# Kernel optimization log

Hardware: AMD Instinct MI355X
Metric: run time of the kernel (lower is better)

Reference implementation:

```python
import jax, jax.numpy as jnp
import numpy as np

M, N, K, C, G = 16384, 131072, 16, 128, 8
EPS_BN = 1e-5


def _bn(x, g, b):
    # inference-mode BatchNorm1d (running_mean=0, running_var=1)
    return x * (g / jnp.sqrt(1.0 + EPS_BN)) + b


def setup_inputs() -> dict:
    key = jax.random.key(0)
    ks = jax.random.split(key, 16)
    f32 = jnp.float32
    s = 0.05
    return {
        "query_feat": jax.random.normal(ks[0], (M, C), f32),
        "context_feat": jax.random.normal(ks[1], (N, C), f32),
        "query_coord": jax.random.normal(ks[2], (M, 3), f32),
        "context_coord": jax.random.normal(ks[3], (N, 3), f32),
        "Wq": jax.random.normal(ks[4], (C, C), f32) * s,
        "bq": jnp.zeros((C,), f32),
        "gq": jnp.ones((C,), f32),
        "betaq": jnp.zeros((C,), f32),
        "Wk": jax.random.normal(ks[5], (C, C), f32) * s,
        "bk": jnp.zeros((C,), f32),
        "gk": jnp.ones((C,), f32),
        "betak": jnp.zeros((C,), f32),
        "Wv": jax.random.normal(ks[6], (C, C), f32) * s,
        "bv": jnp.zeros((C,), f32),
        "Wp1": jax.random.normal(ks[7], (3, C), f32) * s,
        "bp1": jnp.zeros((C,), f32),
        "gp1": jnp.ones((C,), f32),
        "betap1": jnp.zeros((C,), f32),
        "Wp2": jax.random.normal(ks[8], (C, C), f32) * s,
        "bp2": jnp.zeros((C,), f32),
        "Ww1": jax.random.normal(ks[9], (C, G), f32) * s,
        "bw1": jnp.zeros((G,), f32),
        "gw1": jnp.ones((G,), f32),
        "betaw1": jnp.zeros((G,), f32),
        "Ww2": jax.random.normal(ks[10], (G, G), f32) * s,
        "bw2": jnp.zeros((G,), f32),
        "knn_indexes": jax.random.randint(ks[11], (M, K), 0, N, dtype=jnp.int32),
    }


def reference(query_feat, context_feat, query_coord, context_coord,
              Wq, bq, gq, betaq, Wk, bk, gk, betak, Wv, bv,
              Wp1, bp1, gp1, betap1, Wp2, bp2,
              Ww1, bw1, gw1, betaw1, Ww2, bw2, knn_indexes):
    q = jax.nn.relu(_bn(query_feat @ Wq + bq, gq, betaq))              # (M, C)
    k = jax.nn.relu(_bn(context_feat @ Wk + bk, gk, betak))            # (N, C)
    v = context_feat @ Wv + bv                                         # (N, C)

    mask = knn_indexes >= 0                                            # (M, K); -1 = padded neighbor
    idx = jnp.where(mask, knn_indexes, 0)
    mf = mask[..., None].astype(q.dtype)                               # (M, K, 1)

    key_g = k[idx] * mf                                                # (M, K, C) gather (zero row for -1)
    val_g = v[idx] * mf                                                # (M, K, C)
    pos = (context_coord[idx] - query_coord[:, None, :]) * mf          # (M, K, 3) relative position

    # positional-encoding bias branch (pe_bias=True, pe_multiplier=False)
    peb = jax.nn.relu(_bn(pos @ Wp1 + bp1, gp1, betap1)) @ Wp2 + bp2   # (M, K, C)
    rel = key_g - q[:, None, :] + peb                                  # (M, K, C)
    val_g = val_g + peb

    # grouped vector attention weights
    w = jax.nn.relu(_bn(rel @ Ww1 + bw1, gw1, betaw1)) @ Ww2 + bw2     # (M, K, G)
    w = jax.nn.softmax(w, axis=1) * mf                                 # softmax over neighbors, mask padded

    m_, k_ = idx.shape
    c_ = q.shape[-1]
    g_ = w.shape[-1]
    out = jnp.einsum('mkgi,mkg->mgi', val_g.reshape(m_, k_, g_, c_ // g_), w)
    return out.reshape(m_, c_)
```

## Files before the change

kernel.cpp:

```cpp
#include <hip/hip_runtime.h>

#define C 128
#define G 8
#define KNN 16
#define QB 4
#define EPS 1e-5f

typedef unsigned short u16;
typedef __attribute__((ext_vector_type(8))) short short8;
typedef __attribute__((ext_vector_type(4))) float float4v;

union frag_u { short8 v; u16 u[8]; };

__device__ inline u16 f2bf(float f) {
    unsigned u = __builtin_bit_cast(unsigned, f);
    unsigned r = (u + 0x7fffu + ((u >> 16) & 1u)) >> 16;
    return (u16)r;
}
__device__ inline float bf2f(u16 h) {
    unsigned u = ((unsigned)h) << 16;
    return __builtin_bit_cast(float, u);
}

__global__ __launch_bounds__(256) void prep_w(
    const float* __restrict__ Wk, const float* __restrict__ Wv,
    const float* __restrict__ Wq, const float* __restrict__ Wp2,
    const float* __restrict__ Ww1, const float* __restrict__ bp2,
    u16* __restrict__ dst, float* __restrict__ cw1)
{
    const int b = blockIdx.x, t = threadIdx.x;
    if (b < 16) {
        const int mi = b >> 2, qt = b & 3;
        const float* W = mi == 0 ? Wk : mi == 1 ? Wv : mi == 2 ? Wq : Wp2;
        u16* d = dst + mi * 16384;
        for (int e = qt * 4096 + t; e < (qt + 1) * 4096; e += 256) {
            const int k = e >> 7, n = e & 127;
            const int cb = n >> 4, lan = n & 15;
            const int kk = k >> 5, quad = (k >> 3) & 3, j = k & 7;
            d[(((cb * 4 + kk) * 4 + quad) * 16 + lan) * 8 + j] = f2bf(W[e]);
        }
    } else if (b == 16) {
        u16* d = dst + 4 * 16384;
        for (int e = t; e < 4096; e += 256) {
            const int j = e & 7, lan = (e >> 3) & 15;
            const int quad = (e >> 7) & 3, kk = e >> 9;
            const int k = kk * 32 + quad * 8 + j;
            d[e] = lan < 8 ? f2bf(Ww1[k * G + lan]) : (u16)0;
        }
    } else {
        u16* d = dst + 4 * 16384 + 4096;
        for (int e = t; e < 4096; e += 256) d[e] = 0;
        __syncthreads();
#pragma unroll
        for (int it = 0; it < 4; it++) {
            const int k = it * 32 + (t >> 3), g = t & 7;
            float a = 0.f;
            for (int i = 0; i < C; i++)
                a = fmaf(Wp2[k * C + i], Ww1[i * G + g], a);
            const int kk = k >> 5, quad = (k >> 3) & 3, j = k & 7;
            d[((kk * 4 + quad) * 16 + g) * 8 + j] = f2bf(a);
        }
        if (t < G) {
            float a = 0.f;
            for (int i = 0; i < C; i++) a = fmaf(bp2[i], Ww1[i * G + t], a);
            cw1[t] = a;
        }
    }
}

__global__ __launch_bounds__(256) void proj_all(
    const float* __restrict__ Xc, const float* __restrict__ Xq,
    const u16* __restrict__ PWk, const float* __restrict__ bk,
    const float* __restrict__ gk, const float* __restrict__ betak,
    const u16* __restrict__ PWv, const float* __restrict__ bv,
    const u16* __restrict__ PWq, const float* __restrict__ bq,
    const float* __restrict__ gq, const float* __restrict__ betaq,
    const u16* __restrict__ PWw1b,
    u16* __restrict__ vout, u16* __restrict__ Kp, u16* __restrict__ Qp,
    int nkv)
{
    __shared__ u16 Xs[64 * 136];
    const int t = threadIdx.x;
    const int w = t >> 6, l = t & 63;
    const int quad = l >> 4, lan = l & 15;
    const bool isq = (int)blockIdx.x >= nkv;
    const long long row0 = (long long)(isq ? blockIdx.x - nkv : blockIdx.x) * 64;
    const float* X = isq ? Xq : Xc;

    {
        const float4* Xv = (const float4*)(X + row0 * C);
#pragma unroll
        for (int i = 0; i < 8; i++) {
            const int e = t + 256 * i;
            const int r = e >> 5, c4 = e & 31;
            const float4 f = Xv[e];
            uint2 p;
            p.x = (unsigned)f2bf(f.x) | ((unsigned)f2bf(f.y) << 16);
            p.y = (unsigned)f2bf(f.z) | ((unsigned)f2bf(f.w) << 16);
            *(uint2*)(&Xs[r * 136 + c4 * 4]) = p;
        }
    }
    __syncthreads();

    if (!isq) {
        unsigned vp[2][4][2];
        {
            short8 Bf[2][4];
#pragma unroll
            for (int ct = 0; ct < 2; ct++) {
                const int cb = w * 2 + ct;
#pragma unroll
                for (int kk = 0; kk < 4; kk++)
                    Bf[ct][kk] = *(const short8*)(PWv + (((cb * 4 + kk) * 4 + quad) * 16 + lan) * 8);
            }
            float4v acc[2][4];
#pragma unroll
            for (int ct = 0; ct < 2; ct++)
#pragma unroll
                for (int rt = 0; rt < 4; rt++) acc[ct][rt] = (float4v)0.f;
#pragma unroll
            for (int rt = 0; rt < 4; rt++)
#pragma unroll
                for (int kk = 0; kk < 4; kk++) {
                    const short8 A = *(const short8*)(&Xs[(rt * 16 + lan) * 136 + kk * 32 + quad * 8]);
#pragma unroll
                    for (int ct = 0; ct < 2; ct++)
                        acc[ct][rt] = __builtin_amdgcn_mfma_f32_16x16x32_bf16(
                            A, Bf[ct][kk], acc[ct][rt], 0, 0, 0);
                }
#pragma unroll
            for (int ct = 0; ct < 2; ct++) {
                const float bb = bv[w * 32 + ct * 16 + lan];
#pragma unroll
                for (int rt = 0; rt < 4; rt++)
#pragma unroll
                    for (int h = 0; h < 2; h++)
                        vp[ct][rt][h] = (unsigned)f2bf(acc[ct][rt][2 * h] + bb)
                                      | ((unsigned)f2bf(acc[ct][rt][2 * h + 1] + bb) << 16);
            }
        }
        float4v acck[2][4];
        {
            short8 Bf[2][4];
#pragma unroll
            for (int ct = 0; ct < 2; ct++) {
                const int cb = w * 2 + ct;
#pragma unroll
                for (int kk = 0; kk < 4; kk++)
                    Bf[ct][kk] = *(const short8*)(PWk + (((cb * 4 + kk) * 4 + quad) * 16 + lan) * 8);
            }
#pragma unroll
            for (int ct = 0; ct < 2; ct++)
#pragma unroll
                for (int rt = 0; rt < 4; rt++) acck[ct][rt] = (float4v)0.f;
#pragma unroll
            for (int rt = 0; rt < 4; rt++)
#pragma unroll
                for (int kk = 0; kk < 4; kk++) {
                    const short8 A = *(const short8*)(&Xs[(rt * 16 + lan) * 136 + kk * 32 + quad * 8]);
#pragma unroll
                    for (int ct = 0; ct < 2; ct++)
                        acck[ct][rt] = __builtin_amdgcn_mfma_f32_16x16x32_bf16(
                            A, Bf[ct][kk], acck[ct][rt], 0, 0, 0);
                }
        }
        __syncthreads();

#pragma unroll
        for (int ct = 0; ct < 2; ct++) {
            const int cg = w * 32 + ct * 16 + lan;
            const float bb = bk[cg];
            const float sc = gk[cg] * rsqrtf(1.f + EPS);
            const float sh = betak[cg];
#pragma unroll
            for (int rt = 0; rt < 4; rt++)
#pragma unroll
                for (int reg = 0; reg < 4; reg++) {
                    float y = (acck[ct][rt][reg] + bb) * sc + sh;
                    y = y > 0.f ? y : 0.f;
                    Xs[(rt * 16 + quad * 4 + reg) * 136 + cg] = f2bf(y);
                }
        }
        __syncthreads();

        {
            short8 Bw[4];
#pragma unroll
            for (int kk = 0; kk < 4; kk++)
                Bw[kk] = *(const short8*)(PWw1b + ((kk * 4 + quad) * 16 + lan) * 8);
            float4v ka = (float4v)0.f;
#pragma unroll
            for (int kk = 0; kk < 4; kk++) {
                const short8 A = *(const short8*)(&Xs[(w * 16 + lan) * 136 + kk * 32 + quad * 8]);
                ka = __builtin_amdgcn_mfma_f32_16x16x32_bf16(A, Bw[kk], ka, 0, 0, 0);
            }
            if (lan < G) {
#pragma unroll
                for (int reg = 0; reg < 4; reg++)
                    Kp[(row0 + w * 16 + quad * 4 + reg) * G + lan] = f2bf(ka[reg]);
            }
        }
        __syncthreads();

#pragma unroll
        for (int ct = 0; ct < 2; ct++) {
            const int cg = w * 32 + ct * 16 + lan;
#pragma unroll
            for (int rt = 0; rt < 4; rt++)
#pragma unroll
                for (int h = 0; h < 2; h++) {
                    Xs[(rt * 16 + quad * 4 + 2 * h) * 136 + cg]     = (u16)(vp[ct][rt][h] & 0xffffu);
                    Xs[(rt * 16 + quad * 4 + 2 * h + 1) * 136 + cg] = (u16)(vp[ct][rt][h] >> 16);
                }
        }
        __syncthreads();
#pragma unroll
        for (int i = 0; i < 4; i++) {
            const int e = t + 256 * i;
            const int r = e >> 4, cc = (e & 15) * 8;
            *(short8*)(vout + (row0 + r) * C + cc) = *(const short8*)(&Xs[r * 136 + cc]);
        }
    } else {
        float4v acc[2][4];
        {
            short8 Bf[2][4];
#pragma unroll
            for (int ct = 0; ct < 2; ct++) {
                const int cb = w * 2 + ct;
#pragma unroll
                for (int kk = 0; kk < 4; kk++)
                    Bf[ct][kk] = *(const short8*)(PWq + (((cb * 4 + kk) * 4 + quad) * 16 + lan) * 8);
            }
#pragma unroll
            for (int ct = 0; ct < 2; ct++)
#pragma unroll
                for (int rt = 0; rt < 4; rt++) acc[ct][rt] = (float4v)0.f;
#pragma unroll
            for (int rt = 0; rt < 4; rt++)
#pragma unroll
                for (int kk = 0; kk < 4; kk++) {
                    const short8 A = *(const short8*)(&Xs[(rt * 16 + lan) * 136 + kk * 32 + quad * 8]);
#pragma unroll
                    for (int ct = 0; ct < 2; ct++)
                        acc[ct][rt] = __builtin_amdgcn_mfma_f32_16x16x32_bf16(
                            A, Bf[ct][kk], acc[ct][rt], 0, 0, 0);
                }
        }
        __syncthreads();
#pragma unroll
        for (int ct = 0; ct < 2; ct++) {
            const int cg = w * 32 + ct * 16 + lan;
            const float bb = bq[cg];
            const float sc = gq[cg] * rsqrtf(1.f + EPS);
            const float sh = betaq[cg];
#pragma unroll
            for (int rt = 0; rt < 4; rt++)
#pragma unroll
                for (int reg = 0; reg < 4; reg++) {
                    float y = (acc[ct][rt][reg] + bb) * sc + sh;
                    y = y > 0.f ? y : 0.f;
                    Xs[(rt * 16 + quad * 4 + reg) * 136 + cg] = f2bf(y);
                }
        }
        __syncthreads();
        {
            short8 Bw[4];
#pragma unroll
            for (int kk = 0; kk < 4; kk++)
                Bw[kk] = *(const short8*)(PWw1b + ((kk * 4 + quad) * 16 + lan) * 8);
            float4v qa = (float4v)0.f;
#pragma unroll
            for (int kk = 0; kk < 4; kk++) {
                const short8 A = *(const short8*)(&Xs[(w * 16 + lan) * 136 + kk * 32 + quad * 8]);
                qa = __builtin_amdgcn_mfma_f32_16x16x32_bf16(A, Bw[kk], qa, 0, 0, 0);
            }
            if (lan < G) {
#pragma unroll
                for (int reg = 0; reg < 4; reg++)
                    Qp[(row0 + w * 16 + quad * 4 + reg) * G + lan] = f2bf(qa[reg]);
            }
        }
    }
}

__global__ __launch_bounds__(256) void attn6(
    const u16* __restrict__ vbuf, const u16* __restrict__ Kp,
    const u16* __restrict__ Qp,
    const float* __restrict__ qcoord, const float* __restrict__ ccoord,
    const float* __restrict__ Wp1, const float* __restrict__ bp1,
    const float* __restrict__ gp1, const float* __restrict__ betap1,
    const u16* __restrict__ PWp2, const float* __restrict__ bp2,
    const u16* __restrict__ PWp2pb, const float* __restrict__ cw1,
    const float* __restrict__ bw1,
    const float* __restrict__ gw1, const float* __restrict__ betaw1,
    const float* __restrict__ Ww2, const float* __restrict__ bw2,
    const int* __restrict__ knn, float* __restrict__ out)
{
    __shared__ u16   fA[64 * 136];
    __shared__ u16   kgs[64 * G];
    __shared__ float qps[QB * G];
    __shared__ float pebp[64 * G];
    __shared__ float cw1s[G];
    __shared__ float pxs[64], pys[64], pzs[64];
    __shared__ int   idxs[64];
    __shared__ float wl[QB * 16 * G];

    const int t = threadIdx.x;
    const int w = t >> 6, l = t & 63;
    const int quad = l >> 4, lan = l & 15;
    const int m0 = blockIdx.x * QB;
    const int rsub = t >> 4;
    const int c8 = (t & 15) * 8;

    float mfr[4];
    frag_u vg[4];
#pragma unroll
    for (int p = 0; p < 4; p++) {
        const int ii = knn[m0 * KNN + p * 16 + rsub];
        mfr[p] = ii >= 0 ? 1.f : 0.f;
        const size_t i0 = ii >= 0 ? ii : 0;
        vg[p].v = *(const short8*)(vbuf + i0 * C + c8);
    }
    if (t < 64) {
        const int q = t >> 4;
        const int ii = knn[m0 * KNN + t];
        const float mf = ii >= 0 ? 1.f : 0.f;
        const int i0 = ii >= 0 ? ii : 0;
        idxs[t] = ii;
        pxs[t] = (ccoord[i0 * 3 + 0] - qcoord[(m0 + q) * 3 + 0]) * mf;
        pys[t] = (ccoord[i0 * 3 + 1] - qcoord[(m0 + q) * 3 + 1]) * mf;
        pzs[t] = (ccoord[i0 * 3 + 2] - qcoord[(m0 + q) * 3 + 2]) * mf;
        *(short8*)(&kgs[t * G]) = *(const short8*)(Kp + (size_t)i0 * G);
    } else if (t < 68) {
        const int p = t - 64;
        frag_u qv;
        qv.v = *(const short8*)(Qp + (size_t)(m0 + p) * G);
#pragma unroll
        for (int j = 0; j < G; j++) qps[p * G + j] = bf2f(qv.u[j]);
    } else if (t < 76) {
        cw1s[t - 68] = cw1[t - 68];
    }
    __syncthreads();

    {
        const int c = t & 127, hh = t >> 7;
        const float w0 = Wp1[c], w1_ = Wp1[C + c], w2_ = Wp1[2 * C + c];
        const float sc = gp1[c] * rsqrtf(1.f + EPS);
        const float bb = bp1[c], sh = betap1[c];
#pragma unroll
        for (int r2 = 0; r2 < 32; r2++) {
            const int r = hh * 32 + r2;
            float y = fmaf(pxs[r], w0, fmaf(pys[r], w1_, fmaf(pzs[r], w2_, bb)));
            y = y * sc + sh;
            y = y > 0.f ? y : 0.f;
            fA[r * 136 + c] = f2bf(y);
        }
    }
    __syncthreads();

    float4v acc[2][4];
    float4v pp = (float4v)0.f;
    {
        short8 Bf[2][4];
#pragma unroll
        for (int ct = 0; ct < 2; ct++) {
            const int cb = w * 2 + ct;
#pragma unroll
            for (int kk = 0; kk < 4; kk++)
                Bf[ct][kk] = *(const short8*)(PWp2 + (((cb * 4 + kk) * 4 + quad) * 16 + lan) * 8);
        }
#pragma unroll
        for (int ct = 0; ct < 2; ct++)
#pragma unroll
            for (int q = 0; q < 4; q++) acc[ct][q] = (float4v)0.f;
#pragma unroll
        for (int q = 0; q < 4; q++)
#pragma unroll
            for (int kk = 0; kk < 4; kk++) {
                const short8 A = *(const short8*)(&fA[(q * 16 + lan) * 136 + kk * 32 + quad * 8]);
#pragma unroll
                for (int ct = 0; ct < 2; ct++)
                    acc[ct][q] = __builtin_amdgcn_mfma_f32_16x16x32_bf16(
                        A, Bf[ct][kk], acc[ct][q], 0, 0, 0);
            }
#pragma unroll
        for (int kk = 0; kk < 4; kk++) {
            const short8 Bp = *(const short8*)(PWp2pb + ((kk * 4 + quad) * 16 + lan) * 8);
            const short8 A = *(const short8*)(&fA[(w * 16 + lan) * 136 + kk * 32 + quad * 8]);
            pp = __builtin_amdgcn_mfma_f32_16x16x32_bf16(A, Bp, pp, 0, 0, 0);
        }
    }
    __syncthreads();

    {
        const float bb0 = bp2[w * 32 + lan];
        const float bb1 = bp2[w * 32 + 16 + lan];
#pragma unroll
        for (int ct = 0; ct < 2; ct++)
#pragma unroll
            for (int q = 0; q < 4; q++)
#pragma unroll
                for (int reg = 0; reg < 4; reg++)
                    fA[(q * 16 + quad * 4 + reg) * 136 + w * 32 + ct * 16 + lan] =
                        f2bf(acc[ct][q][reg] + (ct ? bb1 : bb0));
        if (lan < G) {
#pragma unroll
            for (int reg = 0; reg < 4; reg++)
                pebp[(w * 16 + quad * 4 + reg) * G + lan] = pp[reg];
        }
    }
    __syncthreads();

    {
#pragma unroll
        for (int p = 0; p < 4; p++) {
            const int r = p * 16 + rsub;
            const float mf = mfr[p];
            frag_u peb, valv;
            peb.v = *(const short8*)(&fA[r * 136 + c8]);
#pragma unroll
            for (int j = 0; j < 8; j++)
                valv.u[j] = f2bf(fmaf(bf2f(vg[p].u[j]), mf, bf2f(peb.u[j])));
            *(short8*)(&fA[r * 136 + c8]) = valv.v;
        }
    }
    if (t < 64) {
        const int q = t >> 4, j = t & 15;
        const float mf = idxs[t] >= 0 ? 1.f : 0.f;
#pragma unroll
        for (int g = 0; g < G; g++) {
            const float L = bf2f(kgs[t * G + g]) * mf - qps[q * G + g]
                          + pebp[t * G + g] + cw1s[g] + bw1[g];
            const float y = L * (gw1[g] * rsqrtf(1.f + EPS)) + betaw1[g];
            wl[q * 128 + j * G + g] = y > 0.f ? y : 0.f;
        }
    }
    __syncthreads();

    if (t < QB * G) {
        const int q = t >> 3, g2 = t & 7;
        float w2c[G];
#pragma unroll
        for (int g = 0; g < G; g++) w2c[g] = Ww2[g * G + g2];
        const float bb = bw2[g2];
        float lg[KNN], mx = -1e30f;
#pragma unroll
        for (int j = 0; j < KNN; j++) {
            float a = bb;
#pragma unroll
            for (int g = 0; g < G; g++) a = fmaf(wl[q * 128 + j * 8 + g], w2c[g], a);
            lg[j] = a;
            mx = fmaxf(mx, a);
        }
        float sum = 0.f;
#pragma unroll
        for (int j = 0; j < KNN; j++) { lg[j] = __expf(lg[j] - mx); sum += lg[j]; }
        const float inv = 1.f / sum;
#pragma unroll
        for (int j = 0; j < KNN; j++) {
            const float mf = idxs[q * 16 + j] >= 0 ? 1.f : 0.f;
            wl[q * 128 + j * 8 + g2] = lg[j] * inv * mf;
        }
    }
    __syncthreads();

#pragma unroll
    for (int i = 0; i < 2; i++) {
        const int e = t + 256 * i;
        const int q = e >> 7, c = e & 127, g = c >> 4;
        float a = 0.f;
#pragma unroll
        for (int j = 0; j < KNN; j++)
            a = fmaf(bf2f(fA[(q * 16 + j) * 136 + c]), wl[q * 128 + j * 8 + g], a);
        out[(size_t)(m0 + q) * C + c] = a;
    }
}

extern "C" void kernel_launch(void* const* d_in, const int* in_sizes, int n_in,
                              void* d_out, int out_size, void* d_ws, size_t ws_size,
                              hipStream_t stream)
{
    const float* query_feat    = (const float*)d_in[0];
    const float* context_feat  = (const float*)d_in[1];
    const float* query_coord   = (const float*)d_in[2];
    const float* context_coord = (const float*)d_in[3];
    const float* Wq    = (const float*)d_in[4];
    const float* bq    = (const float*)d_in[5];
    const float* gq    = (const float*)d_in[6];
    const float* betaq = (const float*)d_in[7];
    const float* Wk    = (const float*)d_in[8];
    const float* bk    = (const float*)d_in[9];
    const float* gk    = (const float*)d_in[10];
    const float* betak = (const float*)d_in[11];
    const float* Wv    = (const float*)d_in[12];
    const float* bv    = (const float*)d_in[13];
    const float* Wp1   = (const float*)d_in[14];
    const float* bp1   = (const float*)d_in[15];
    const float* gp1   = (const float*)d_in[16];
    const float* betap1= (const float*)d_in[17];
    const float* Wp2   = (const float*)d_in[18];
    const float* bp2   = (const float*)d_in[19];
    const float* Ww1   = (const float*)d_in[20];
    const float* bw1   = (const float*)d_in[21];
    const float* gw1   = (const float*)d_in[22];
    const float* betaw1= (const float*)d_in[23];
    const float* Ww2   = (const float*)d_in[24];
    const float* bw2   = (const float*)d_in[25];
    const int*   knn   = (const int*)d_in[26];

    const int M = in_sizes[0] / C;
    const int N = in_sizes[1] / C;

    u16* vb = (u16*)d_ws;
    u16* Kp = vb + (size_t)N * C;
    u16* Qp = Kp + (size_t)N * G;
    u16* pw = Qp + (size_t)M * G;
    u16* pWk    = pw;
    u16* pWv    = pw + 16384;
    u16* pWq    = pw + 2 * 16384;
    u16* pWp2   = pw + 3 * 16384;
    u16* pWw1b  = pw + 4 * 16384;
    u16* pWp2pb = pw + 4 * 16384 + 4096;
    float* cw1  = (float*)(pw + 4 * 16384 + 2 * 4096);

    prep_w<<<18, 256, 0, stream>>>(Wk, Wv, Wq, Wp2, Ww1, bp2, pw, cw1);
    proj_all<<<N / 64 + M / 64, 256, 0, stream>>>(
        context_feat, query_feat,
        pWk, bk, gk, betak, pWv, bv,
        pWq, bq, gq, betaq, pWw1b,
        vb, Kp, Qp, N / 64);
    attn6<<<M / QB, 256, 0, stream>>>(vb, Kp, Qp, query_coord, context_coord,
                                      Wp1, bp1, gp1, betap1, pWp2, bp2,
                                      pWp2pb, cw1, bw1, gw1, betaw1, Ww2, bw2,
                                      knn, (float*)d_out);
}
```

Measured before the change: 218.8 us.

## Compute positional first layer with MFMA and pack bf16 conversions

The 3->128 positional-encoding linear layer in the attention kernel now runs as a zero-padded bf16 MFMA, using a new prepacked Wp1 fragment built by an extra prep block, in place of scalar FMAs over LDS coordinates. Shared memory is overlaid so the position buffer, pebp and wl share one region, which adds a sync. Scalar bf16 rounding is replaced by packed float2->bf16 intrinsics in several places. This cuts VALU work and LDS footprint, at the cost of padding waste in the MFMA and bf16 rounding of the coordinates and Wp1.

```diff
diff --git a/kernel.cpp b/kernel.cpp
--- a/kernel.cpp
+++ b/kernel.cpp
@@ -1,4 +1,5 @@
 #include <hip/hip_runtime.h>
+#include <hip/hip_bf16.h>
 
 #define C 128
 #define G 8
@@ -10,7 +11,7 @@
 typedef __attribute__((ext_vector_type(8))) short short8;
 typedef __attribute__((ext_vector_type(4))) float float4v;
 
-union frag_u { short8 v; u16 u[8]; };
+union frag_u { short8 v; u16 u[8]; unsigned d[4]; };
 
 __device__ inline u16 f2bf(float f) {
     unsigned u = __builtin_bit_cast(unsigned, f);
@@ -21,11 +22,18 @@
     unsigned u = ((unsigned)h) << 16;
     return __builtin_bit_cast(float, u);
 }
+__device__ inline unsigned pkbf(float a, float b) {
+    __hip_bfloat162 h = __float22bfloat162_rn(float2{a, b});
+    unsigned r;
+    __builtin_memcpy(&r, &h, 4);
+    return r;
+}
 
 __global__ __launch_bounds__(256) void prep_w(
     const float* __restrict__ Wk, const float* __restrict__ Wv,
     const float* __restrict__ Wq, const float* __restrict__ Wp2,
-    const float* __restrict__ Ww1, const float* __restrict__ bp2,
+    const float* __restrict__ Ww1, const float* __restrict__ Wp1,
+    const float* __restrict__ bp2,
     u16* __restrict__ dst, float* __restrict__ cw1)
 {
     const int b = blockIdx.x, t = threadIdx.x;
@@ -47,7 +55,7 @@
             const int k = kk * 32 + quad * 8 + j;
             d[e] = lan < 8 ? f2bf(Ww1[k * G + lan]) : (u16)0;
         }
-    } else {
+    } else if (b == 17) {
         u16* d = dst + 4 * 16384 + 4096;
         for (int e = t; e < 4096; e += 256) d[e] = 0;
         __syncthreads();
@@ -64,6 +72,16 @@
             float a = 0.f;
             for (int i = 0; i < C; i++) a = fmaf(bp2[i], Ww1[i * G + t], a);
             cw1[t] = a;
+        }
+    } else {
+        u16* d = dst + 4 * 16384 + 2 * 4096;
+        for (int e = t; e < 4096; e += 256) d[e] = 0;
+        __syncthreads();
+        if (t < 128) {
+            const int cb = t >> 4, lan = t & 15;
+#pragma unroll
+            for (int j = 0; j < 3; j++)
+                d[(cb * 64 + lan) * 8 + j] = f2bf(Wp1[j * C + cb * 16 + lan]);
         }
     }
 }
@@ -79,7 +97,7 @@
     u16* __restrict__ vout, u16* __restrict__ Kp, u16* __restrict__ Qp,
     int nkv)
 {
-    __shared__ u16 Xs[64 * 136];
+    __shared__ __align__(16) u16 Xs[64 * 136];
     const int t = threadIdx.x;
     const int w = t >> 6, l = t & 63;
     const int quad = l >> 4, lan = l & 15;
@@ -95,8 +113,8 @@
             const int r = e >> 5, c4 = e & 31;
             const float4 f = Xv[e];
             uint2 p;
-            p.x = (unsigned)f2bf(f.x) | ((unsigned)f2bf(f.y) << 16);
-            p.y = (unsigned)f2bf(f.z) | ((unsigned)f2bf(f.w) << 16);
+            p.x = pkbf(f.x, f.y);
+            p.y = pkbf(f.z, f.w);
             *(uint2*)(&Xs[r * 136 + c4 * 4]) = p;
         }
     }
@@ -135,8 +153,7 @@
                 for (int rt = 0; rt < 4; rt++)
 #pragma unroll
                     for (int h = 0; h < 2; h++)
-                        vp[ct][rt][h] = (unsigned)f2bf(acc[ct][rt][2 * h] + bb)
-                                      | ((unsigned)f2bf(acc[ct][rt][2 * h + 1] + bb) << 16);
+                        vp[ct][rt][h] = pkbf(acc[ct][rt][2 * h] + bb, acc[ct][rt][2 * h + 1] + bb);
             }
         }
         float4v acck[2][4];
@@ -283,11 +300,11 @@
     }
 }
 
-__global__ __launch_bounds__(256) void attn6(
+__global__ __launch_bounds__(256) void attn7(
     const u16* __restrict__ vbuf, const u16* __restrict__ Kp,
     const u16* __restrict__ Qp,
     const float* __restrict__ qcoord, const float* __restrict__ ccoord,
-    const float* __restrict__ Wp1, const float* __restrict__ bp1,
+    const u16* __restrict__ PWp1b, const float* __restrict__ bp1,
     const float* __restrict__ gp1, const float* __restrict__ betap1,
     const u16* __restrict__ PWp2, const float* __restrict__ bp2,
     const u16* __restrict__ PWp2pb, const float* __restrict__ cw1,
@@ -296,14 +313,15 @@
     const float* __restrict__ Ww2, const float* __restrict__ bw2,
     const int* __restrict__ knn, float* __restrict__ out)
 {
-    __shared__ u16   fA[64 * 136];
-    __shared__ u16   kgs[64 * G];
+    __shared__ __align__(16) u16 fA[64 * 136];
+    __shared__ __align__(16) float ovl[1024];
+    __shared__ __align__(16) u16 kgs[64 * G];
     __shared__ float qps[QB * G];
-    __shared__ float pebp[64 * G];
     __shared__ float cw1s[G];
-    __shared__ float pxs[64], pys[64], pzs[64];
     __shared__ int   idxs[64];
-    __shared__ float wl[QB * 16 * G];
+    u16*   posb = (u16*)ovl;
+    float* pebp = ovl;
+    float* wl   = ovl + 512;
 
     const int t = threadIdx.x;
     const int w = t >> 6, l = t & 63;
@@ -327,9 +345,16 @@
         const float mf = ii >= 0 ? 1.f : 0.f;
         const int i0 = ii >= 0 ? ii : 0;
         idxs[t] = ii;
-        pxs[t] = (ccoord[i0 * 3 + 0] - qcoord[(m0 + q) * 3 + 0]) * mf;
-        pys[t] = (ccoord[i0 * 3 + 1] - qcoord[(m0 + q) * 3 + 1]) * mf;
-        pzs[t] = (ccoord[i0 * 3 + 2] - qcoord[(m0 + q) * 3 + 2]) * mf;
+        const float px = (ccoord[i0 * 3 + 0] - qcoord[(m0 + q) * 3 + 0]) * mf;
+        const float py = (ccoord[i0 * 3 + 1] - qcoord[(m0 + q) * 3 + 1]) * mf;
+        const float pz = (ccoord[i0 * 3 + 2] - qcoord[(m0 + q) * 3 + 2]) * mf;
+        frag_u z; z.v = (short8)0;
+        z.u[0] = f2bf(px); z.u[1] = f2bf(py); z.u[2] = f2bf(pz);
+        const short8 zz = (short8)0;
+        *(short8*)(&posb[t * 32])      = z.v;
+        *(short8*)(&posb[t * 32 + 8])  = zz;
+        *(short8*)(&posb[t * 32 + 16]) = zz;
+        *(short8*)(&posb[t * 32 + 24]) = zz;
         *(short8*)(&kgs[t * G]) = *(const short8*)(Kp + (size_t)i0 * G);
     } else if (t < 68) {
         const int p = t - 64;
@@ -343,17 +368,36 @@
     __syncthreads();
 
     {
-        const int c = t & 127, hh = t >> 7;
-        const float w0 = Wp1[c], w1_ = Wp1[C + c], w2_ = Wp1[2 * C + c];
-        const float sc = gp1[c] * rsqrtf(1.f + EPS);
-        const float bb = bp1[c], sh = betap1[c];
-#pragma unroll
-        for (int r2 = 0; r2 < 32; r2++) {
-            const int r = hh * 32 + r2;
-            float y = fmaf(pxs[r], w0, fmaf(pys[r], w1_, fmaf(pzs[r], w2_, bb)));
-            y = y * sc + sh;
-            y = y > 0.f ? y : 0.f;
-            fA[r * 136 + c] = f2bf(y);
+        short8 Bp[2];
+#pragma unroll
+        for (int ct = 0; ct < 2; ct++)
+            Bp[ct] = *(const short8*)(PWp1b + (((w * 2 + ct) * 4 + quad) * 16 + lan) * 8);
+        float4v ha[2][4];
+#pragma unroll
+        for (int ct = 0; ct < 2; ct++)
+#pragma unroll
+            for (int q = 0; q < 4; q++) ha[ct][q] = (float4v)0.f;
+#pragma unroll
+        for (int q = 0; q < 4; q++) {
+            const short8 A = *(const short8*)(&posb[(q * 16 + lan) * 32 + quad * 8]);
+#pragma unroll
+            for (int ct = 0; ct < 2; ct++)
+                ha[ct][q] = __builtin_amdgcn_mfma_f32_16x16x32_bf16(A, Bp[ct], ha[ct][q], 0, 0, 0);
+        }
+        __syncthreads();
+#pragma unroll
+        for (int ct = 0; ct < 2; ct++) {
+            const int col = w * 32 + ct * 16 + lan;
+            const float sc = gp1[col] * rsqrtf(1.f + EPS);
+            const float bb = bp1[col], sh = betap1[col];
+#pragma unroll
+            for (int q = 0; q < 4; q++)
+#pragma unroll
+                for (int reg = 0; reg < 4; reg++) {
+                    float y = (ha[ct][q][reg] + bb) * sc + sh;
+                    y = y > 0.f ? y : 0.f;
+                    fA[(q * 16 + quad * 4 + reg) * 136 + col] = f2bf(y);
+                }
         }
     }
     __syncthreads();
@@ -419,8 +463,9 @@
             frag_u peb, valv;
             peb.v = *(const short8*)(&fA[r * 136 + c8]);
 #pragma unroll
-            for (int j = 0; j < 8; j++)
-                valv.u[j] = f2bf(fmaf(bf2f(vg[p].u[j]), mf, bf2f(peb.u[j])));
+            for (int h = 0; h < 4; h++)
+                valv.d[h] = pkbf(fmaf(bf2f(vg[p].u[2 * h]),     mf, bf2f(peb.u[2 * h])),
+                                 fmaf(bf2f(vg[p].u[2 * h + 1]), mf, bf2f(peb.u[2 * h + 1])));
             *(short8*)(&fA[r * 136 + c8]) = valv.v;
         }
     }
@@ -521,16 +566,17 @@
     u16* pWp2   = pw + 3 * 16384;
     u16* pWw1b  = pw + 4 * 16384;
     u16* pWp2pb = pw + 4 * 16384 + 4096;
-    float* cw1  = (float*)(pw + 4 * 16384 + 2 * 4096);
-
-    prep_w<<<18, 256, 0, stream>>>(Wk, Wv, Wq, Wp2, Ww1, bp2, pw, cw1);
+    u16* pWp1b  = pw + 4 * 16384 + 2 * 4096;
+    float* cw1  = (float*)(pw + 4 * 16384 + 3 * 4096);
+
+    prep_w<<<19, 256, 0, stream>>>(Wk, Wv, Wq, Wp2, Ww1, Wp1, bp2, pw, cw1);
     proj_all<<<N / 64 + M / 64, 256, 0, stream>>>(
         context_feat, query_feat,
         pWk, bk, gk, betak, pWv, bv,
         pWq, bq, gq, betaq, pWw1b,
         vb, Kp, Qp, N / 64);
-    attn6<<<M / QB, 256, 0, stream>>>(vb, Kp, Qp, query_coord, context_coord,
-                                      Wp1, bp1, gp1, betap1, pWp2, bp2,
+    attn7<<<M / QB, 256, 0, stream>>>(vb, Kp, Qp, query_coord, context_coord,
+                                      pWp1b, bp1, gp1, betap1, pWp2, bp2,
                                       pWp2pb, cw1, bw1, gw1, betaw1, Ww2, bw2,
                                       knn, (float*)d_out);
 }
```

After: 220.0 us. About the same (+0.5%).

## Restructure attention kernel to one query per wave without block barriers

Applied to the files above, without the earlier changes.

The attention kernel now gives each wavefront a single query with its own shared-memory slice, so every __syncthreads is gone and softmax reductions use wave shuffles. The first positional layer (3->C linear plus BN and bias) is folded into a prepacked bf16 weight tile and computed with one MFMA per column tile, replacing scalar FMAs. Packed bf16 conversion intrinsics replace manual rounding in proj_all. Trade-offs: the Wp2 B fragments are now loaded from global memory per wave instead of being amortised across queries, and the wave-local LDS use relies on implicit in-wave ordering.

```diff
diff --git a/kernel.cpp b/kernel.cpp
--- a/kernel.cpp
+++ b/kernel.cpp
@@ -1,16 +1,16 @@
 #include <hip/hip_runtime.h>
+#include <hip/hip_bf16.h>
 
 #define C 128
 #define G 8
 #define KNN 16
-#define QB 4
 #define EPS 1e-5f
 
 typedef unsigned short u16;
 typedef __attribute__((ext_vector_type(8))) short short8;
 typedef __attribute__((ext_vector_type(4))) float float4v;
 
-union frag_u { short8 v; u16 u[8]; };
+union frag_u { short8 v; u16 u[8]; unsigned d[4]; };
 
 __device__ inline u16 f2bf(float f) {
     unsigned u = __builtin_bit_cast(unsigned, f);
@@ -21,11 +21,19 @@
     unsigned u = ((unsigned)h) << 16;
     return __builtin_bit_cast(float, u);
 }
+__device__ inline unsigned pkbf(float a, float b) {
+    __hip_bfloat162 h = __float22bfloat162_rn(float2{a, b});
+    unsigned r;
+    __builtin_memcpy(&r, &h, 4);
+    return r;
+}
 
 __global__ __launch_bounds__(256) void prep_w(
     const float* __restrict__ Wk, const float* __restrict__ Wv,
     const float* __restrict__ Wq, const float* __restrict__ Wp2,
-    const float* __restrict__ Ww1, const float* __restrict__ bp2,
+    const float* __restrict__ Ww1, const float* __restrict__ Wp1,
+    const float* __restrict__ bp1, const float* __restrict__ gp1,
+    const float* __restrict__ betap1, const float* __restrict__ bp2,
     u16* __restrict__ dst, float* __restrict__ cw1)
 {
     const int b = blockIdx.x, t = threadIdx.x;
@@ -47,7 +55,7 @@
             const int k = kk * 32 + quad * 8 + j;
             d[e] = lan < 8 ? f2bf(Ww1[k * G + lan]) : (u16)0;
         }
-    } else {
+    } else if (b == 17) {
         u16* d = dst + 4 * 16384 + 4096;
         for (int e = t; e < 4096; e += 256) d[e] = 0;
         __syncthreads();
@@ -64,6 +72,19 @@
             float a = 0.f;
             for (int i = 0; i < C; i++) a = fmaf(bp2[i], Ww1[i * G + t], a);
             cw1[t] = a;
+        }
+    } else {
+        u16* d = dst + 4 * 16384 + 2 * 4096;
+        for (int e = t; e < 4096; e += 256) d[e] = 0;
+        __syncthreads();
+        if (t < 128) {
+            const int cb = t >> 4, lan = t & 15;
+            const int col = cb * 16 + lan;
+            const float s = gp1[col] * rsqrtf(1.f + EPS);
+#pragma unroll
+            for (int j = 0; j < 3; j++)
+                d[(cb * 64 + lan) * 8 + j] = f2bf(Wp1[j * C + col] * s);
+            d[(cb * 64 + lan) * 8 + 3] = f2bf(bp1[col] * s + betap1[col]);
         }
     }
 }
@@ -79,7 +100,7 @@
     u16* __restrict__ vout, u16* __restrict__ Kp, u16* __restrict__ Qp,
     int nkv)
 {
-    __shared__ u16 Xs[64 * 136];
+    __shared__ __align__(16) u16 Xs[64 * 136];
     const int t = threadIdx.x;
     const int w = t >> 6, l = t & 63;
     const int quad = l >> 4, lan = l & 15;
@@ -95,8 +116,8 @@
             const int r = e >> 5, c4 = e & 31;
             const float4 f = Xv[e];
             uint2 p;
-            p.x = (unsigned)f2bf(f.x) | ((unsigned)f2bf(f.y) << 16);
-            p.y = (unsigned)f2bf(f.z) | ((unsigned)f2bf(f.w) << 16);
+            p.x = pkbf(f.x, f.y);
+            p.y = pkbf(f.z, f.w);
             *(uint2*)(&Xs[r * 136 + c4 * 4]) = p;
         }
     }
@@ -135,8 +156,7 @@
                 for (int rt = 0; rt < 4; rt++)
 #pragma unroll
                     for (int h = 0; h < 2; h++)
-                        vp[ct][rt][h] = (unsigned)f2bf(acc[ct][rt][2 * h] + bb)
-                                      | ((unsigned)f2bf(acc[ct][rt][2 * h + 1] + bb) << 16);
+                        vp[ct][rt][h] = pkbf(acc[ct][rt][2 * h] + bb, acc[ct][rt][2 * h + 1] + bb);
             }
         }
         float4v acck[2][4];
@@ -283,12 +303,11 @@
     }
 }
 
-__global__ __launch_bounds__(256) void attn6(
+__global__ __launch_bounds__(256) void attn8(
     const u16* __restrict__ vbuf, const u16* __restrict__ Kp,
     const u16* __restrict__ Qp,
     const float* __restrict__ qcoord, const float* __restrict__ ccoord,
-    const float* __restrict__ Wp1, const float* __restrict__ bp1,
-    const float* __restrict__ gp1, const float* __restrict__ betap1,
+    const u16* __restrict__ PWp1b,
     const u16* __restrict__ PWp2, const float* __restrict__ bp2,
     const u16* __restrict__ PWp2pb, const float* __restrict__ cw1,
     const float* __restrict__ bw1,
@@ -296,184 +315,154 @@
     const float* __restrict__ Ww2, const float* __restrict__ bw2,
     const int* __restrict__ knn, float* __restrict__ out)
 {
-    __shared__ u16   fA[64 * 136];
-    __shared__ u16   kgs[64 * G];
-    __shared__ float qps[QB * G];
-    __shared__ float pebp[64 * G];
-    __shared__ float cw1s[G];
-    __shared__ float pxs[64], pys[64], pzs[64];
-    __shared__ int   idxs[64];
-    __shared__ float wl[QB * 16 * G];
-
+    __shared__ __align__(16) unsigned char smem[4 * 5120];
     const int t = threadIdx.x;
     const int w = t >> 6, l = t & 63;
     const int quad = l >> 4, lan = l & 15;
-    const int m0 = blockIdx.x * QB;
-    const int rsub = t >> 4;
-    const int c8 = (t & 15) * 8;
-
-    float mfr[4];
+    const int m = blockIdx.x * 4 + w;
+
+    u16*   h1v = (u16*)(smem + w * 5120);
+    u16*   kg  = h1v + 16 * 136;
+    float* wl  = (float*)(kg + 16 * 8);
+
+    int ii = -1;
+    if (l < KNN) ii = knn[m * KNN + l];
+    const int myrow = l >> 2;
+    const int idxr = __shfl(ii, myrow);
+    const float mfrow = idxr >= 0 ? 1.f : 0.f;
+    const size_t r0 = idxr >= 0 ? (size_t)idxr : 0;
+    const int c0 = (l & 3) * 32;
+
     frag_u vg[4];
 #pragma unroll
-    for (int p = 0; p < 4; p++) {
-        const int ii = knn[m0 * KNN + p * 16 + rsub];
-        mfr[p] = ii >= 0 ? 1.f : 0.f;
-        const size_t i0 = ii >= 0 ? ii : 0;
-        vg[p].v = *(const short8*)(vbuf + i0 * C + c8);
-    }
-    if (t < 64) {
-        const int q = t >> 4;
-        const int ii = knn[m0 * KNN + t];
+    for (int h = 0; h < 4; h++)
+        vg[h].v = *(const short8*)(vbuf + r0 * C + c0 + h * 8);
+
+    float px = 0.f, py = 0.f, pz = 0.f;
+    if (l < KNN) {
+        const int i0 = ii >= 0 ? ii : 0;
         const float mf = ii >= 0 ? 1.f : 0.f;
-        const int i0 = ii >= 0 ? ii : 0;
-        idxs[t] = ii;
-        pxs[t] = (ccoord[i0 * 3 + 0] - qcoord[(m0 + q) * 3 + 0]) * mf;
-        pys[t] = (ccoord[i0 * 3 + 1] - qcoord[(m0 + q) * 3 + 1]) * mf;
-        pzs[t] = (ccoord[i0 * 3 + 2] - qcoord[(m0 + q) * 3 + 2]) * mf;
-        *(short8*)(&kgs[t * G]) = *(const short8*)(Kp + (size_t)i0 * G);
-    } else if (t < 68) {
-        const int p = t - 64;
-        frag_u qv;
-        qv.v = *(const short8*)(Qp + (size_t)(m0 + p) * G);
-#pragma unroll
-        for (int j = 0; j < G; j++) qps[p * G + j] = bf2f(qv.u[j]);
-    } else if (t < 76) {
-        cw1s[t - 68] = cw1[t - 68];
-    }
-    __syncthreads();
-
-    {
-        const int c = t & 127, hh = t >> 7;
-        const float w0 = Wp1[c], w1_ = Wp1[C + c], w2_ = Wp1[2 * C + c];
-        const float sc = gp1[c] * rsqrtf(1.f + EPS);
-        const float bb = bp1[c], sh = betap1[c];
-#pragma unroll
-        for (int r2 = 0; r2 < 32; r2++) {
-            const int r = hh * 32 + r2;
-            float y = fmaf(pxs[r], w0, fmaf(pys[r], w1_, fmaf(pzs[r], w2_, bb)));
-            y = y * sc + sh;
-            y = y > 0.f ? y : 0.f;
-            fA[r * 136 + c] = f2bf(y);
-        }
-    }
-    __syncthreads();
-
-    float4v acc[2][4];
+        px = (ccoord[i0 * 3 + 0] - qcoord[m * 3 + 0]) * mf;
+        py = (ccoord[i0 * 3 + 1] - qcoord[m * 3 + 1]) * mf;
+        pz = (ccoord[i0 * 3 + 2] - qcoord[m * 3 + 2]) * mf;
+        *(short8*)(&kg[l * G]) = *(const short8*)(Kp + (size_t)i0 * G);
+    }
+
+    frag_u A0; A0.v = (short8)0;
+    if (quad == 0) {
+        A0.u[0] = f2bf(px); A0.u[1] = f2bf(py); A0.u[2] = f2bf(pz);
+        A0.u[3] = 0x3F80;
+    }
+    float4v h1a[8];
+#pragma unroll
+    for (int ct = 0; ct < 8; ct++) {
+        const short8 Bp = *(const short8*)(PWp1b + ((ct * 4 + quad) * 16 + lan) * 8);
+        h1a[ct] = __builtin_amdgcn_mfma_f32_16x16x32_bf16(A0.v, Bp, (float4v)0.f, 0, 0, 0);
+    }
+#pragma unroll
+    for (int ct = 0; ct < 8; ct++)
+#pragma unroll
+        for (int reg = 0; reg < 4; reg++) {
+            const float y = h1a[ct][reg] > 0.f ? h1a[ct][reg] : 0.f;
+            h1v[(quad * 4 + reg) * 136 + ct * 16 + lan] = f2bf(y);
+        }
+
+    float4v pacc[8];
+#pragma unroll
+    for (int ct = 0; ct < 8; ct++) pacc[ct] = (float4v)0.f;
     float4v pp = (float4v)0.f;
-    {
-        short8 Bf[2][4];
-#pragma unroll
-        for (int ct = 0; ct < 2; ct++) {
-            const int cb = w * 2 + ct;
-#pragma unroll
-            for (int kk = 0; kk < 4; kk++)
-                Bf[ct][kk] = *(const short8*)(PWp2 + (((cb * 4 + kk) * 4 + quad) * 16 + lan) * 8);
-        }
-#pragma unroll
-        for (int ct = 0; ct < 2; ct++)
-#pragma unroll
-            for (int q = 0; q < 4; q++) acc[ct][q] = (float4v)0.f;
-#pragma unroll
-        for (int q = 0; q < 4; q++)
-#pragma unroll
-            for (int kk = 0; kk < 4; kk++) {
-                const short8 A = *(const short8*)(&fA[(q * 16 + lan) * 136 + kk * 32 + quad * 8]);
-#pragma unroll
-                for (int ct = 0; ct < 2; ct++)
-                    acc[ct][q] = __builtin_amdgcn_mfma_f32_16x16x32_bf16(
-                        A, Bf[ct][kk], acc[ct][q], 0, 0, 0);
-            }
-#pragma unroll
-        for (int kk = 0; kk < 4; kk++) {
-            const short8 Bp = *(const short8*)(PWp2pb + ((kk * 4 + quad) * 16 + lan) * 8);
-            const short8 A = *(const short8*)(&fA[(w * 16 + lan) * 136 + kk * 32 + quad * 8]);
-            pp = __builtin_amdgcn_mfma_f32_16x16x32_bf16(A, Bp, pp, 0, 0, 0);
-        }
-    }
-    __syncthreads();
-
-    {
-        const float bb0 = bp2[w * 32 + lan];
-        const float bb1 = bp2[w * 32 + 16 + lan];
-#pragma unroll
-        for (int ct = 0; ct < 2; ct++)
-#pragma unroll
-            for (int q = 0; q < 4; q++)
-#pragma unroll
-                for (int reg = 0; reg < 4; reg++)
-                    fA[(q * 16 + quad * 4 + reg) * 136 + w * 32 + ct * 16 + lan] =
-                        f2bf(acc[ct][q][reg] + (ct ? bb1 : bb0));
-        if (lan < G) {
-#pragma unroll
-            for (int reg = 0; reg < 4; reg++)
-                pebp[(w * 16 + quad * 4 + reg) * G + lan] = pp[reg];
-        }
-    }
-    __syncthreads();
-
-    {
-#pragma unroll
-        for (int p = 0; p < 4; p++) {
-            const int r = p * 16 + rsub;
-            const float mf = mfr[p];
-            frag_u peb, valv;
-            peb.v = *(const short8*)(&fA[r * 136 + c8]);
-#pragma unroll
-            for (int j = 0; j < 8; j++)
-                valv.u[j] = f2bf(fmaf(bf2f(vg[p].u[j]), mf, bf2f(peb.u[j])));
-            *(short8*)(&fA[r * 136 + c8]) = valv.v;
-        }
-    }
-    if (t < 64) {
-        const int q = t >> 4, j = t & 15;
-        const float mf = idxs[t] >= 0 ? 1.f : 0.f;
-#pragma unroll
-        for (int g = 0; g < G; g++) {
-            const float L = bf2f(kgs[t * G + g]) * mf - qps[q * G + g]
-                          + pebp[t * G + g] + cw1s[g] + bw1[g];
-            const float y = L * (gw1[g] * rsqrtf(1.f + EPS)) + betaw1[g];
-            wl[q * 128 + j * G + g] = y > 0.f ? y : 0.f;
-        }
-    }
-    __syncthreads();
-
-    if (t < QB * G) {
-        const int q = t >> 3, g2 = t & 7;
-        float w2c[G];
-#pragma unroll
-        for (int g = 0; g < G; g++) w2c[g] = Ww2[g * G + g2];
-        const float bb = bw2[g2];
-        float lg[KNN], mx = -1e30f;
-#pragma unroll
-        for (int j = 0; j < KNN; j++) {
-            float a = bb;
-#pragma unroll
-            for (int g = 0; g < G; g++) a = fmaf(wl[q * 128 + j * 8 + g], w2c[g], a);
-            lg[j] = a;
-            mx = fmaxf(mx, a);
-        }
-        float sum = 0.f;
-#pragma unroll
-        for (int j = 0; j < KNN; j++) { lg[j] = __expf(lg[j] - mx); sum += lg[j]; }
-        const float inv = 1.f / sum;
-#pragma unroll
-        for (int j = 0; j < KNN; j++) {
-            const float mf = idxs[q * 16 + j] >= 0 ? 1.f : 0.f;
-            wl[q * 128 + j * 8 + g2] = lg[j] * inv * mf;
-        }
-    }
-    __syncthreads();
-
-#pragma unroll
-    for (int i = 0; i < 2; i++) {
-        const int e = t + 256 * i;
-        const int q = e >> 7, c = e & 127, g = c >> 4;
-        float a = 0.f;
-#pragma unroll
-        for (int j = 0; j < KNN; j++)
-            a = fmaf(bf2f(fA[(q * 16 + j) * 136 + c]), wl[q * 128 + j * 8 + g], a);
-        out[(size_t)(m0 + q) * C + c] = a;
-    }
+#pragma unroll
+    for (int kk = 0; kk < 4; kk++) {
+        const short8 A = *(const short8*)(&h1v[lan * 136 + kk * 32 + quad * 8]);
+#pragma unroll
+        for (int ct = 0; ct < 8; ct++) {
+            const short8 Bf = *(const short8*)(PWp2 + (((ct * 4 + kk) * 4 + quad) * 16 + lan) * 8);
+            pacc[ct] = __builtin_amdgcn_mfma_f32_16x16x32_bf16(A, Bf, pacc[ct], 0, 0, 0);
+        }
+        const short8 Bpp = *(const short8*)(PWp2pb + ((kk * 4 + quad) * 16 + lan) * 8);
+        pp = __builtin_amdgcn_mfma_f32_16x16x32_bf16(A, Bpp, pp, 0, 0, 0);
+    }
+
+#pragma unroll
+    for (int ct = 0; ct < 8; ct++) {
+        const float bb = bp2[ct * 16 + lan];
+#pragma unroll
+        for (int reg = 0; reg < 4; reg++)
+            h1v[(quad * 4 + reg) * 136 + ct * 16 + lan] = f2bf(pacc[ct][reg] + bb);
+    }
+
+#pragma unroll
+    for (int h = 0; h < 4; h++) {
+        frag_u pe, va;
+        pe.v = *(const short8*)(&h1v[myrow * 136 + c0 + h * 8]);
+#pragma unroll
+        for (int x = 0; x < 4; x++)
+            va.d[x] = pkbf(fmaf(bf2f(vg[h].u[2 * x]),     mfrow, bf2f(pe.u[2 * x])),
+                           fmaf(bf2f(vg[h].u[2 * x + 1]), mfrow, bf2f(pe.u[2 * x + 1])));
+        *(short8*)(&h1v[myrow * 136 + c0 + h * 8]) = va.v;
+    }
+
+    const int g = lan & 7;
+    const float qpg  = bf2f(Qp[(size_t)m * G + g]);
+    const float cst  = cw1[g] + bw1[g];
+    const float sg   = gw1[g] * rsqrtf(1.f + EPS);
+    const float shg  = betaw1[g];
+    const float mfq0 = __shfl(ii, quad * 4 + 0) >= 0 ? 1.f : 0.f;
+    const float mfq1 = __shfl(ii, quad * 4 + 1) >= 0 ? 1.f : 0.f;
+    const float mfq2 = __shfl(ii, quad * 4 + 2) >= 0 ? 1.f : 0.f;
+    const float mfq3 = __shfl(ii, quad * 4 + 3) >= 0 ? 1.f : 0.f;
+    const float mfj[4] = {mfq0, mfq1, mfq2, mfq3};
+    if (lan < G) {
+#pragma unroll
+        for (int reg = 0; reg < 4; reg++) {
+            const int row = quad * 4 + reg;
+            const float kv = bf2f(kg[row * G + g]);
+            const float L = kv * mfj[reg] - qpg + pp[reg] + cst;
+            const float y = L * sg + shg;
+            wl[row * G + g] = y > 0.f ? y : 0.f;
+        }
+    }
+
+    float w2c[G];
+#pragma unroll
+    for (int gg = 0; gg < G; gg++) w2c[gg] = Ww2[gg * G + g];
+    const float bb2 = bw2[g];
+    float lg[4];
+#pragma unroll
+    for (int reg = 0; reg < 4; reg++) {
+        const int row = quad * 4 + reg;
+        float a = bb2;
+#pragma unroll
+        for (int gg = 0; gg < G; gg++) a = fmaf(wl[row * G + gg], w2c[gg], a);
+        lg[reg] = a;
+    }
+    float mx = fmaxf(fmaxf(lg[0], lg[1]), fmaxf(lg[2], lg[3]));
+    mx = fmaxf(mx, __shfl_xor(mx, 16));
+    mx = fmaxf(mx, __shfl_xor(mx, 32));
+    float e[4], s = 0.f;
+#pragma unroll
+    for (int reg = 0; reg < 4; reg++) { e[reg] = __expf(lg[reg] - mx); s += e[reg]; }
+    s += __shfl_xor(s, 16);
+    s += __shfl_xor(s, 32);
+    const float inv = 1.f / s;
+    if (lan < G) {
+#pragma unroll
+        for (int reg = 0; reg < 4; reg++)
+            wl[(quad * 4 + reg) * G + g] = e[reg] * inv * mfj[reg];
+    }
+
+    const int cpa = 2 * l;
+    const int gout = l >> 3;
+    float a0 = 0.f, a1 = 0.f;
+#pragma unroll
+    for (int j = 0; j < KNN; j++) {
+        const unsigned pv = *(const unsigned*)(&h1v[j * 136 + cpa]);
+        const float wj = wl[j * G + gout];
+        a0 = fmaf(bf2f((u16)(pv & 0xffffu)), wj, a0);
+        a1 = fmaf(bf2f((u16)(pv >> 16)), wj, a1);
+    }
+    float2 o; o.x = a0; o.y = a1;
+    *(float2*)(out + (size_t)m * C + cpa) = o;
 }
 
 extern "C" void kernel_launch(void* const* d_in, const int* in_sizes, int n_in,
@@ -521,16 +510,18 @@
     u16* pWp2   = pw + 3 * 16384;
     u16* pWw1b  = pw + 4 * 16384;
     u16* pWp2pb = pw + 4 * 16384 + 4096;
-    float* cw1  = (float*)(pw + 4 * 16384 + 2 * 4096);
-
-    prep_w<<<18, 256, 0, stream>>>(Wk, Wv, Wq, Wp2, Ww1, bp2, pw, cw1);
+    u16* pWp1b  = pw + 4 * 16384 + 2 * 4096;
+    float* cw1  = (float*)(pw + 4 * 16384 + 3 * 4096);
+
+    prep_w<<<19, 256, 0, stream>>>(Wk, Wv, Wq, Wp2, Ww1, Wp1, bp1, gp1, betap1,
+                                   bp2, pw, cw1);
     proj_all<<<N / 64 + M / 64, 256, 0, stream>>>(
         context_feat, query_feat,
         pWk, bk, gk, betak, pWv, bv,
         pWq, bq, gq, betaq, pWw1b,
         vb, Kp, Qp, N / 64);
-    attn6<<<M / QB, 256, 0, stream>>>(vb, Kp, Qp, query_coord, context_coord,
-                                      Wp1, bp1, gp1, betap1, pWp2, bp2,
-                                      pWp2pb, cw1, bw1, gw1, betaw1, Ww2, bw2,
-                                      knn, (float*)d_out);
-}
+    attn8<<<M / 4, 256, 0, stream>>>(vb, Kp, Qp, query_coord, context_coord,
+                                     pWp1b, pWp2, bp2,
+                                     pWp2pb, cw1, bw1, gw1, betaw1, Ww2, bw2,
+                                     knn, (float*)d_out);
+}
```

New measurement: 224.6 us. 1.03x slower.
